# Kernel optimization log

Measured on AMD Instinct MI355X. Metric: run time of the kernel, lower is better.

Reference implementation:

```python
import jax, jax.numpy as jnp
import numpy as np

BETA = 1.0  # commitment loss weight (beta=1.0 in VQKD.__init__)

def l2norm(x, eps=1e-12):
    return x / jnp.maximum(jnp.linalg.norm(x, axis=-1, keepdims=True), eps)

def setup_inputs() -> dict:
    key = jax.random.key(0)
    k0, k1, k2, k3 = jax.random.split(key, 4)
    B, N, D_ENC, D_CODE, K = 8, 4096, 768, 32, 8192
    std = 0.02  # trunc_normal_(std=0.02) init of task layers
    return {
        "features": jax.random.normal(k0, (B, N, D_ENC), jnp.float32),
        "enc_w1": jax.random.normal(k1, (D_ENC, D_ENC), jnp.float32) * std,
        "enc_b1": jnp.zeros((D_ENC,), jnp.float32),
        "enc_w2": jax.random.normal(k2, (D_ENC, D_CODE), jnp.float32) * std,
        "enc_b2": jnp.zeros((D_CODE,), jnp.float32),
        "codebook": jax.random.normal(k3, (K, D_CODE), jnp.float32),
    }

def reference(features, enc_w1, enc_b1, enc_w2, enc_b2, codebook):
    # encode_task_layer: Linear -> Tanh -> Linear (run in fp32, as in the autocast-disabled block)
    z = jnp.tanh(features @ enc_w1 + enc_b1) @ enc_w2 + enc_b2          # [B, N, C]
    # NormEMAVectorQuantizer: l2-normalize tokens and (EMA-normalized) codebook
    z = l2norm(z)
    emb = l2norm(codebook)                                              # [K, C]
    # squared euclidean distances  ||z||^2 - 2 z.e + ||e||^2  -> [B, N, K]
    d = (jnp.sum(z * z, axis=-1, keepdims=True)
         - 2.0 * jnp.einsum('bnc,kc->bnk', z, emb)
         + jnp.sum(emb * emb, axis=-1))
    idx = jnp.argmin(d, axis=-1)                                        # [B, N] int32
    z_q_raw = emb[idx]                                                  # gather [B, N, C]
    loss = BETA * jnp.mean((jax.lax.stop_gradient(z_q_raw) - z) ** 2)   # commitment loss
    z_q = z + jax.lax.stop_gradient(z_q_raw - z)                        # straight-through
    return z_q, loss, idx
```

## Files before the change

### kernel.cpp

```cpp
#include <hip/hip_runtime.h>
#include <hip/hip_bf16.h>
#include <cstdint>
#include <cstddef>


namespace {
constexpr int TOKENS = 8 * 4096;
constexpr int DENC   = 768;
constexpr int DC     = 32;
constexpr int KC     = 8192;
constexpr int BM = 128, BN = 128, BK = 32;
constexpr int NSTEP = DENC / BK;
constexpr int NT    = DENC / BN;
constexpr float WSCALE = 1024.0f;
constexpr float HSCALE = 512.0f;
constexpr float SSCALE = 512.0f;
constexpr int SCH = 256;
}

typedef _Float16 f16x8 __attribute__((ext_vector_type(8)));
typedef float    f32x4 __attribute__((ext_vector_type(4)));

__device__ inline void split2(float v, _Float16& h, _Float16& l) {
  h = (_Float16)v;
  l = (_Float16)(v - (float)h);
}

__device__ inline void gload_lds16(const void* g, void* l) {
  __builtin_amdgcn_global_load_lds(
      (const __attribute__((address_space(1))) void*)g,
      (__attribute__((address_space(3))) void*)l, 16, 0, 0);
}

__global__ void ksplitW(const float* __restrict__ W1,
                        _Float16* __restrict__ Wh, _Float16* __restrict__ Wl) {
  int n = blockIdx.y;
  int k = blockIdx.x * 256 + threadIdx.x;
  float w = W1[(size_t)k * DENC + n] * WSCALE;
  _Float16 h, l; split2(w, h, l);
  Wh[(size_t)n * DENC + k] = h;
  Wl[(size_t)n * DENC + k] = l;
}

__global__ void ksplitW2(const float* __restrict__ W2,
                         _Float16* __restrict__ W2h, _Float16* __restrict__ W2l) {
  int i = blockIdx.x * 256 + threadIdx.x;
  int k = i >> 5, c = i & 31;
  float w = W2[(size_t)k * DC + c] * WSCALE;
  _Float16 h, l; split2(w, h, l);
  W2h[(size_t)c * DENC + k] = h;
  W2l[(size_t)c * DENC + k] = l;
}

__global__ void knorm_codes(const float* __restrict__ cb,
                            float* __restrict__ embn, float* __restrict__ se2,
                            _Float16* __restrict__ Eh, _Float16* __restrict__ El) {
  int t = blockIdx.x * blockDim.x + threadIdx.x;
  int k = t >> 5, c = t & 31;
  float v = cb[(size_t)k * DC + c];
  float ss = v * v;
  #pragma unroll
  for (int m = 16; m >= 1; m >>= 1) ss += __shfl_xor(ss, m, 32);
  float nrm = fmaxf(sqrtf(ss), 1e-12f);
  float vn = v / nrm;
  embn[(size_t)k * DC + c] = vn;
  _Float16 h, l; split2(vn * SSCALE, h, l);
  Eh[(size_t)k * DC + c] = h;
  El[(size_t)k * DC + c] = l;
  float s2 = vn * vn;
  #pragma unroll
  for (int m = 16; m >= 1; m >>= 1) s2 += __shfl_xor(s2, m, 32);
  if (c == 0) se2[k] = s2 * (SSCALE * SSCALE);
}

__global__ __launch_bounds__(256, 4)
void kfused(const float* __restrict__ X,
            const _Float16* __restrict__ Wh, const _Float16* __restrict__ Wl,
            const float* __restrict__ bias1,
            const _Float16* __restrict__ W2h, const _Float16* __restrict__ W2l,
            float* __restrict__ zpart) {
  __shared__ __align__(16) char smem[34816];
  char*     AsB = smem;
  _Float16* Bsm = (_Float16*)(smem + 16384);
  float (*Hs)[68] = (float(*)[68])smem;

  const int bid = blockIdx.x;
  const int xcd = bid & 7;
  const int w   = bid >> 3;
  const int n_t = w % 6;
  const int m_t = xcd * 32 + w / 6;
  const int m0 = m_t * BM, n0 = n_t * BN;

  const int t    = threadIdx.x;
  const int lane = t & 63;
  const int wv   = t >> 6;
  const int wm   = wv >> 1, wn = wv & 1;
  const int lrow = lane & 15;
  const int lgrp = lane >> 4;

  const int ae = (lane & 1) ^ ((lane >> 3) & 1);
  const float* xsrcA = X + (size_t)(m0 + wv * 32 + (lane >> 1)) * DENC + ae * 4;
  const _Float16* bsrc[2] = {
    Wh + (size_t)(n0 + (wv & 1) * 64 + lane) * DENC,
    Wl + (size_t)(n0 + (wv & 1) * 64 + lane) * DENC };
  const int bko_half = wv >> 1;

  f32x4 acc[4][4];
  #pragma unroll
  for (int i = 0; i < 4; ++i)
    #pragma unroll
    for (int j = 0; j < 4; ++j) acc[i][j] = (f32x4)0.0f;

  char* BsB = (char*)Bsm;
  auto stage = [&](int s) {
    const int k0 = s * BK;
    #pragma unroll
    for (int r = 0; r < 4; ++r)
      gload_lds16(xsrcA + k0 + r * 8, AsB + r * 4096 + wv * 1024);
    #pragma unroll
    for (int r = 0; r < 4; ++r) {
      const int pl = r >> 1;
      const int ko = (r & 1) * 2 + bko_half;
      gload_lds16(bsrc[pl] + k0 + ko * 8, BsB + r * 4096 + wv * 1024);
    }
  };

  stage(0);
  for (int s = 0; s < NSTEP; ++s) {
    __syncthreads();

    f16x8 fah[4], fal[4];
    #pragma unroll
    for (int mf = 0; mf < 4; ++mf) {
      const int row = wm * 64 + mf * 16 + lrow;
      const int b   = (row >> 2) & 1;
      const char* base = AsB + lgrp * 4096 + row * 32;
      float4 u = *(const float4*)(base + ((0 ^ b) << 4));
      float4 v = *(const float4*)(base + ((1 ^ b) << 4));
      float va[8] = {u.x, u.y, u.z, u.w, v.x, v.y, v.z, v.w};
      f16x8 hh, ll;
      #pragma unroll
      for (int e = 0; e < 8; ++e) { _Float16 h, l; split2(va[e], h, l); hh[e] = h; ll[e] = l; }
      fah[mf] = hh; fal[mf] = ll;
    }

    #pragma unroll
    for (int nf = 0; nf < 4; ++nf) {
      const int col = wn * 64 + nf * 16 + lrow;
      f16x8 nbh = *(const f16x8*)&Bsm[((0 * 4 + lgrp) * BN + col) * 8];
      f16x8 nbl = *(const f16x8*)&Bsm[((1 * 4 + lgrp) * BN + col) * 8];
      #pragma unroll
      for (int mf = 0; mf < 4; ++mf) {
        acc[mf][nf] = __builtin_amdgcn_mfma_f32_16x16x32_f16(fah[mf], nbh, acc[mf][nf], 0, 0, 0);
        acc[mf][nf] = __builtin_amdgcn_mfma_f32_16x16x32_f16(fah[mf], nbl, acc[mf][nf], 0, 0, 0);
        acc[mf][nf] = __builtin_amdgcn_mfma_f32_16x16x32_f16(fal[mf], nbh, acc[mf][nf], 0, 0, 0);
      }
    }

    __syncthreads();
    if (s + 1 < NSTEP) stage(s + 1);
  }

  {
    float bv[4];
    #pragma unroll
    for (int nf = 0; nf < 4; ++nf) bv[nf] = bias1[n0 + wn * 64 + nf * 16 + lrow];
    #pragma unroll
    for (int mf = 0; mf < 4; ++mf)
      #pragma unroll
      for (int nf = 0; nf < 4; ++nf)
        #pragma unroll
        for (int r = 0; r < 4; ++r)
          acc[mf][nf][r] = tanhf(acc[mf][nf][r] * (1.0f / WSCALE) + bv[nf]);
  }

  f32x4 zacc[2][2];
  #pragma unroll
  for (int i = 0; i < 2; ++i)
    #pragma unroll
    for (int j = 0; j < 2; ++j) zacc[i][j] = (f32x4)0.0f;

  #pragma unroll
  for (int h = 0; h < 2; ++h) {
    __syncthreads();
    if (wn == h) {
      #pragma unroll
      for (int mf = 0; mf < 4; ++mf)
        #pragma unroll
        for (int nf = 0; nf < 4; ++nf)
          #pragma unroll
          for (int r = 0; r < 4; ++r)
            Hs[wm * 64 + mf * 16 + lgrp * 4 + r][nf * 16 + lrow] = acc[mf][nf][r];
    }
    __syncthreads();
    #pragma unroll
    for (int ks = 0; ks < 2; ++ks) {
      const int koct = ks * 4 + lgrp;
      f16x8 bfh[2], bfl[2];
      #pragma unroll
      for (int nf = 0; nf < 2; ++nf) {
        const int c = nf * 16 + lrow;
        const size_t kg = (size_t)c * DENC + n0 + h * 64 + koct * 8;
        bfh[nf] = *(const f16x8*)&W2h[kg];
        bfl[nf] = *(const f16x8*)&W2l[kg];
      }
      #pragma unroll
      for (int mf = 0; mf < 2; ++mf) {
        const float* hp = &Hs[wv * 32 + mf * 16 + lrow][koct * 8];
        float4 u = *(const float4*)hp, v = *(const float4*)(hp + 4);
        float va[8] = {u.x, u.y, u.z, u.w, v.x, v.y, v.z, v.w};
        f16x8 hh, ll;
        #pragma unroll
        for (int e = 0; e < 8; ++e) { _Float16 hx, lx; split2(va[e] * HSCALE, hx, lx); hh[e] = hx; ll[e] = lx; }
        #pragma unroll
        for (int nf = 0; nf < 2; ++nf) {
          zacc[mf][nf] = __builtin_amdgcn_mfma_f32_16x16x32_f16(hh, bfh[nf], zacc[mf][nf], 0, 0, 0);
          zacc[mf][nf] = __builtin_amdgcn_mfma_f32_16x16x32_f16(hh, bfl[nf], zacc[mf][nf], 0, 0, 0);
          zacc[mf][nf] = __builtin_amdgcn_mfma_f32_16x16x32_f16(ll, bfh[nf], zacc[mf][nf], 0, 0, 0);
        }
      }
    }
  }

  float* zp = zpart + (size_t)n_t * TOKENS * DC;
  #pragma unroll
  for (int mf = 0; mf < 2; ++mf)
    #pragma unroll
    for (int r = 0; r < 4; ++r) {
      const int row = m0 + wv * 32 + mf * 16 + lgrp * 4 + r;
      #pragma unroll
      for (int nf = 0; nf < 2; ++nf)
        zp[(size_t)row * DC + nf * 16 + lrow] = zacc[mf][nf][r];
    }
}

__global__ void kreduce(const float* __restrict__ zpart, const float* __restrict__ b2,
                        float* __restrict__ zn) {
  int t = blockIdx.x * blockDim.x + threadIdx.x;
  int c = t & 31;
  float s = 0.0f;
  #pragma unroll
  for (int nt = 0; nt < NT; ++nt) s += zpart[(size_t)nt * TOKENS * DC + t];
  float z = s * (1.0f / (HSCALE * WSCALE)) + b2[c];
  float ss = z * z;
  #pragma unroll
  for (int m = 16; m >= 1; m >>= 1) ss += __shfl_xor(ss, m, 32);
  float nrm = fmaxf(sqrtf(ss), 1e-12f);
  zn[t] = z / nrm;
}

__device__ inline unsigned long long packkey(float d, int idx) {
  unsigned int u = __float_as_uint(d);
  u = (u & 0x80000000u) ? ~u : (u | 0x80000000u);
  return ((unsigned long long)u << 32) | (unsigned int)idx;
}

__global__ __launch_bounds__(256, 4)
void ksearch(const float* __restrict__ zn, const _Float16* __restrict__ Eh,
             const _Float16* __restrict__ El, const float* __restrict__ se2,
             unsigned long long* __restrict__ keys) {
  __shared__ __align__(16) _Float16 Bh[4][SCH][8], Bl[4][SCH][8];
  __shared__ float ce2[SCH];
  const int t = threadIdx.x, lane = t & 63, wv = t >> 6;
  const int tb  = blockIdx.x * 256 + wv * 64;
  const int cb0 = blockIdx.y * 1024;
  const int lr = lane & 15, ko = lane >> 4;

  f16x8 azh[4], azl[4];
  #pragma unroll
  for (int m = 0; m < 4; ++m) {
    const float* zp = zn + (size_t)(tb + m * 16 + lr) * DC + ko * 8;
    float4 u = *(const float4*)zp, v = *(const float4*)(zp + 4);
    float vals[8] = {u.x, u.y, u.z, u.w, v.x, v.y, v.z, v.w};
    f16x8 hh, ll;
    #pragma unroll
    for (int e = 0; e < 8; ++e) {
      _Float16 h, l; split2(vals[e] * SSCALE, h, l);
      hh[e] = h; ll[e] = l;
    }
    azh[m] = hh; azl[m] = ll;
  }

  float best[4][4]; int bi[4][4];
  #pragma unroll
  for (int m = 0; m < 4; ++m)
    #pragma unroll
    for (int r = 0; r < 4; ++r) { best[m][r] = 3.4e38f; bi[m][r] = 0; }

  f16x8 pb[8]; float pe2;

  for (int ch = 0; ch < 4; ++ch) {
    const int cb = cb0 + ch * SCH;
    #pragma unroll
    for (int it = 0; it < 8; ++it) {
      const _Float16* src = (it < 4) ? Eh : El;
      pb[it] = *(const f16x8*)&src[(size_t)(cb + t) * DC + (it & 3) * 8];
    }
    pe2 = se2[cb + t];
    __syncthreads();
    #pragma unroll
    for (int it = 0; it < 8; ++it) {
      _Float16 (*B)[SCH][8] = (it < 4) ? Bh : Bl;
      *(f16x8*)&B[it & 3][t][0] = pb[it];
    }
    ce2[t] = pe2;
    __syncthreads();

    #pragma unroll 4
    for (int f = 0; f < SCH / 16; ++f) {
      f16x8 bh = *(const f16x8*)&Bh[ko][f * 16 + lr][0];
      f16x8 bl = *(const f16x8*)&Bl[ko][f * 16 + lr][0];
      float e2v = ce2[f * 16 + lr];
      int  code = cb + f * 16 + lr;
      #pragma unroll
      for (int m = 0; m < 4; ++m) {
        f32x4 a = (f32x4)0.0f;
        a = __builtin_amdgcn_mfma_f32_16x16x32_f16(azh[m], bh, a, 0, 0, 0);
        a = __builtin_amdgcn_mfma_f32_16x16x32_f16(azh[m], bl, a, 0, 0, 0);
        a = __builtin_amdgcn_mfma_f32_16x16x32_f16(azl[m], bh, a, 0, 0, 0);
        #pragma unroll
        for (int r = 0; r < 4; ++r) {
          float d = fmaf(-2.0f, a[r], e2v);
          bool c = d < best[m][r];
          best[m][r] = c ? d : best[m][r];
          bi[m][r]   = c ? code : bi[m][r];
        }
      }
    }
  }

  #pragma unroll
  for (int m = 0; m < 4; ++m)
    #pragma unroll
    for (int r = 0; r < 4; ++r) {
      float bd = best[m][r]; int ix = bi[m][r];
      #pragma unroll
      for (int s = 1; s < 16; s <<= 1) {
        float od = __shfl_xor(bd, s);
        int   oi = __shfl_xor(ix, s);
        if (od < bd || (od == bd && oi < ix)) { bd = od; ix = oi; }
      }
      if ((lane & 15) == 0) {
        int token = tb + m * 16 + (lane >> 4) * 4 + r;
        atomicMin(&keys[token], packkey(bd, ix));
      }
    }
}

__global__ __launch_bounds__(1024)
void kfinal(const unsigned long long* __restrict__ keys,
            const float* __restrict__ zn, const float* __restrict__ embn,
            float* __restrict__ zq, float* __restrict__ loss,
            float* __restrict__ oidx) {
  __shared__ float red[32];
  int t = blockIdx.x * blockDim.x + threadIdx.x;
  int tok = t >> 5, c = t & 31;
  unsigned long long key = keys[tok];
  int idx = (int)(unsigned int)(key & 0xFFFFFFFFull);
  float q = embn[(size_t)idx * DC + c];
  float z = zn[t];
  zq[t] = z + (q - z);
  float d = q - z;
  float ss = d * d;
  #pragma unroll
  for (int m = 16; m >= 1; m >>= 1) ss += __shfl_xor(ss, m, 32);
  if (c == 0) {
    red[threadIdx.x >> 5] = ss;
    oidx[tok] = (float)idx;
  }
  __syncthreads();
  if (threadIdx.x < 32) {
    float v = red[threadIdx.x];
    #pragma unroll
    for (int m = 16; m >= 1; m >>= 1) v += __shfl_xor(v, m, 32);
    if (threadIdx.x == 0)
      atomicAdd(loss, v * (1.0f / (float)(TOKENS * DC)));
  }
}

extern "C" void kernel_launch(void* const* d_in, const int* in_sizes, int n_in,
                              void* d_out, int out_size, void* d_ws, size_t ws_size,
                              hipStream_t stream) {
  const float* X   = (const float*)d_in[0];
  const float* W1  = (const float*)d_in[1];
  const float* B1  = (const float*)d_in[2];
  const float* W2  = (const float*)d_in[3];
  const float* B2  = (const float*)d_in[4];
  const float* CB  = (const float*)d_in[5];

  float* out  = (float*)d_out;
  float* zq   = out;
  float* loss = out + (size_t)TOKENS * DC;
  float* oidx = loss + 1;

  char* ws = (char*)d_ws;
  size_t off = 0;
  float* zpart = (float*)(ws + off); off += (size_t)NT * TOKENS * DC * 4;
  float* zn   = (float*)(ws + off); off += (size_t)TOKENS * DC * 4;
  float* embn = (float*)(ws + off); off += (size_t)KC * DC * 4;
  float* se2  = (float*)(ws + off); off += (size_t)KC * 4;
  _Float16* Eh = (_Float16*)(ws + off); off += (size_t)KC * DC * 2;
  _Float16* El = (_Float16*)(ws + off); off += (size_t)KC * DC * 2;
  unsigned long long* keys = (unsigned long long*)(ws + off);
  off += (size_t)TOKENS * 8;
  _Float16* W2h = (_Float16*)(ws + off); off += (size_t)DC * DENC * 2;
  _Float16* W2l = (_Float16*)(ws + off); off += (size_t)DC * DENC * 2;
  _Float16* W1h = (_Float16*)zn;
  _Float16* W1l = W1h + (size_t)DENC * DENC;

  hipMemsetAsync(loss, 0, sizeof(float), stream);
  hipMemsetAsync(keys, 0xFF, (size_t)TOKENS * 8, stream);

  ksplitW<<<dim3(DENC / 256, DENC), 256, 0, stream>>>(W1, W1h, W1l);
  ksplitW2<<<(DENC * DC) / 256, 256, 0, stream>>>(W2, W2h, W2l);
  knorm_codes<<<(KC * DC) / 256, 256, 0, stream>>>(CB, embn, se2, Eh, El);
  kfused<<<(TOKENS / BM) * (DENC / BN), 256, 0, stream>>>(X, W1h, W1l, B1, W2h, W2l, zpart);
  kreduce<<<TOKENS * DC / 256, 256, 0, stream>>>(zpart, B2, zn);
  ksearch<<<dim3(TOKENS / 256, KC / 1024), 256, 0, stream>>>(zn, Eh, El, se2, keys);
  kfinal<<<TOKENS * DC / 1024, 1024, 0, stream>>>(keys, zn, embn, zq, loss, oidx);
}
```

Before: 262.9 us.

## Double-buffer A tile in LDS and prefetch B through registers

The A tile is now double-buffered in LDS, so the next step's global-to-LDS load is issued before computing on the current buffer. The B tile is prefetched into registers and written into its single LDS buffer after a barrier. This is meant to overlap global load latency with the MFMA work. In exchange it uses more LDS, lowers the occupancy hint from 4 to 3 blocks, adds a second barrier per step, and drops the XOR swizzle on A, which may bring back LDS bank conflicts.

```diff
diff --git a/kernel.cpp b/kernel.cpp
--- a/kernel.cpp
+++ b/kernel.cpp
@@ -73,16 +73,15 @@
   if (c == 0) se2[k] = s2 * (SSCALE * SSCALE);
 }
 
-__global__ __launch_bounds__(256, 4)
+__global__ __launch_bounds__(256, 3)
 void kfused(const float* __restrict__ X,
             const _Float16* __restrict__ Wh, const _Float16* __restrict__ Wl,
             const float* __restrict__ bias1,
             const _Float16* __restrict__ W2h, const _Float16* __restrict__ W2l,
             float* __restrict__ zpart) {
-  __shared__ __align__(16) char smem[34816];
-  char*     AsB = smem;
-  _Float16* Bsm = (_Float16*)(smem + 16384);
+  __shared__ __align__(16) char smem[49152];
   float (*Hs)[68] = (float(*)[68])smem;
+  char* Breg = smem + 32768;
 
   const int bid = blockIdx.x;
   const int xcd = bid & 7;
@@ -98,8 +97,7 @@
   const int lrow = lane & 15;
   const int lgrp = lane >> 4;
 
-  const int ae = (lane & 1) ^ ((lane >> 3) & 1);
-  const float* xsrcA = X + (size_t)(m0 + wv * 32 + (lane >> 1)) * DENC + ae * 4;
+  const float* xsrcA = X + (size_t)(m0 + wv * 32 + (lane >> 1)) * DENC + (lane & 1) * 4;
   const _Float16* bsrc[2] = {
     Wh + (size_t)(n0 + (wv & 1) * 64 + lane) * DENC,
     Wl + (size_t)(n0 + (wv & 1) * 64 + lane) * DENC };
@@ -111,32 +109,40 @@
     #pragma unroll
     for (int j = 0; j < 4; ++j) acc[i][j] = (f32x4)0.0f;
 
-  char* BsB = (char*)Bsm;
-  auto stage = [&](int s) {
-    const int k0 = s * BK;
+  auto stageA = [&](int s, int buf) {
     #pragma unroll
     for (int r = 0; r < 4; ++r)
-      gload_lds16(xsrcA + k0 + r * 8, AsB + r * 4096 + wv * 1024);
-    #pragma unroll
-    for (int r = 0; r < 4; ++r) {
-      const int pl = r >> 1;
-      const int ko = (r & 1) * 2 + bko_half;
-      gload_lds16(bsrc[pl] + k0 + ko * 8, BsB + r * 4096 + wv * 1024);
-    }
+      gload_lds16(xsrcA + s * BK + r * 8, smem + buf * 16384 + r * 4096 + wv * 1024);
   };
 
-  stage(0);
+  stageA(0, 0);
+  #pragma unroll
+  for (int r = 0; r < 4; ++r) {
+    const int pl = r >> 1, ko = (r & 1) * 2 + bko_half;
+    gload_lds16(bsrc[pl] + ko * 8, Breg + r * 4096 + wv * 1024);
+  }
+  __syncthreads();
+
+  f16x8 pb[4];
   for (int s = 0; s < NSTEP; ++s) {
-    __syncthreads();
-
+    const bool more = (s + 1 < NSTEP);
+    if (more) {
+      stageA(s + 1, (s + 1) & 1);
+      #pragma unroll
+      for (int r = 0; r < 4; ++r) {
+        const int pl = r >> 1, ko = (r & 1) * 2 + bko_half;
+        pb[r] = *(const f16x8*)(bsrc[pl] + (s + 1) * BK + ko * 8);
+      }
+    }
+
+    const char* abase = smem + (size_t)(s & 1) * 16384;
     f16x8 fah[4], fal[4];
     #pragma unroll
     for (int mf = 0; mf < 4; ++mf) {
       const int row = wm * 64 + mf * 16 + lrow;
-      const int b   = (row >> 2) & 1;
-      const char* base = AsB + lgrp * 4096 + row * 32;
-      float4 u = *(const float4*)(base + ((0 ^ b) << 4));
-      float4 v = *(const float4*)(base + ((1 ^ b) << 4));
+      const char* p = abase + lgrp * 4096 + row * 32;
+      float4 u = *(const float4*)p;
+      float4 v = *(const float4*)(p + 16);
       float va[8] = {u.x, u.y, u.z, u.w, v.x, v.y, v.z, v.w};
       f16x8 hh, ll;
       #pragma unroll
@@ -144,6 +150,7 @@
       fah[mf] = hh; fal[mf] = ll;
     }
 
+    const _Float16* Bsm = (const _Float16*)Breg;
     #pragma unroll
     for (int nf = 0; nf < 4; ++nf) {
       const int col = wn * 64 + nf * 16 + lrow;
@@ -158,7 +165,13 @@
     }
 
     __syncthreads();
-    if (s + 1 < NSTEP) stage(s + 1);
+
+    if (more) {
+      #pragma unroll
+      for (int r = 0; r < 4; ++r)
+        *(f16x8*)(Breg + r * 4096 + wv * 1024 + lane * 16) = pb[r];
+    }
+    __syncthreads();
   }
 
   {
```

Result: slower. 269.7 us (+2.6%).
